# Kernel tuning notes

Measured on AMD Instinct MI355X. Metric: run time of the kernel, lower is better.

Reference implementation:

```python
import jax, jax.numpy as jnp
import numpy as np

N_NODES = 307
U = 100          # gru units / GAT out dim
D_IN = 3         # per-node input features
F_IN = U + D_IN  # 103, GATv2 input dim
NEG_SLOPE = 0.2


def setup_inputs() -> dict:
    key = jax.random.key(0)
    ks = jax.random.split(key, 12)
    B, E = 256, 4096
    inputs = jax.random.normal(ks[0], (B, N_NODES * D_IN), dtype=jnp.float32)
    state = jax.random.normal(ks[1], (B, N_NODES * U), dtype=jnp.float32)
    src = jax.random.randint(ks[2], (E,), 0, N_NODES, dtype=jnp.int32)
    dst = jax.random.randint(ks[3], (E,), 0, N_NODES, dtype=jnp.int32)
    def glorot(k, shape):
        lim = float(np.sqrt(6.0 / (shape[0] + shape[1])))
        return jax.random.uniform(k, shape, jnp.float32, -lim, lim)
    return {
        "inputs": inputs, "state": state, "src": src, "dst": dst,
        "Wl": glorot(ks[4], (F_IN, U)),        # GATv2 lin_l (source)
        "Wr": glorot(ks[5], (F_IN, U)),        # GATv2 lin_r (target)
        "att": jax.random.normal(ks[6], (U,), jnp.float32) * 0.1,
        "gat_bias": jnp.zeros((U,), jnp.float32),
        "bias_gc": jnp.zeros((U,), jnp.float32),   # self.bias_1 added in _gc3
        "W_gru1": glorot(ks[7], (F_IN, 2 * U)),    # GRULinear(100,200)
        "b_gru1": jnp.zeros((2 * U,), jnp.float32),
        "W_gru2": glorot(ks[8], (F_IN, U)),        # GRULinear(100,100)
        "b_gru2": jnp.zeros((U,), jnp.float32),
    }


def _gru_linear(inputs, hidden, W, b):
    # cat((inputs[B,N,3], hidden[B,N,U]), -1) @ W + b
    B = hidden.shape[0]
    x = jnp.concatenate([inputs.reshape(B, N_NODES, D_IN),
                         hidden.reshape(B, N_NODES, U)], axis=2)
    return jnp.einsum('bnf,fo->bno', x, W) + b


def _gatv2(x, src, dst, Wl, Wr, att, gat_bias):
    # x: (B, N, F_IN); PyG GATv2Conv with heads=1, add_self_loops=True
    loops = jnp.arange(N_NODES, dtype=src.dtype)
    s = jnp.concatenate([src, loops])
    d = jnp.concatenate([dst, loops])
    xl = jnp.einsum('bnf,fu->bnu', x, Wl)  # source transform
    xr = jnp.einsum('bnf,fu->bnu', x, Wr)  # target transform

    def per_sample(xl_b, xr_b):
        m = xl_b[s]                                        # (E', U)
        e = jax.nn.leaky_relu(m + xr_b[d], NEG_SLOPE) @ att  # (E',)
        emax = jax.ops.segment_max(e, d, num_segments=N_NODES)
        ex = jnp.exp(e - emax[d])
        denom = jax.ops.segment_sum(ex, d, num_segments=N_NODES)
        alpha = ex / denom[d]
        return jax.ops.segment_sum(alpha[:, None] * m, d, num_segments=N_NODES)

    out = jax.vmap(per_sample)(xl, xr)  # (B, N, U)
    return out + gat_bias


def reference(inputs, state, src, dst, Wl, Wr, att, gat_bias, bias_gc,
              W_gru1, b_gru1, W_gru2, b_gru2):
    B = state.shape[0]
    # _gc3: cat([state, inputs]) -> GATv2 per sample -> + bias_1
    x = jnp.concatenate([state.reshape(B, N_NODES, U),
                         inputs.reshape(B, N_NODES, D_IN)], axis=2)
    st = _gatv2(x, src, dst, Wl, Wr, att, gat_bias) + bias_gc
    st = st.reshape(B, N_NODES * U)
    # GRU gating
    value = jax.nn.sigmoid(_gru_linear(inputs, st, W_gru1, b_gru1))  # (B,N,2U)
    r, u = jnp.split(value, 2, axis=-1)
    r = r.reshape(B, N_NODES * U)
    u = u.reshape(B, N_NODES * U)
    c = jnp.tanh(_gru_linear(inputs, r * st, W_gru2, b_gru2)).reshape(B, N_NODES * U)
    return u * st + (1.0 - u) * c
```

## Files before the change

kernel.cpp:

```cpp
#include <hip/hip_runtime.h>
#include <math.h>

#define NN 307
#define UU 100
#define DD 3
#define UP 104
#define UNIT_W 14336
#define HCAP 2560
#define GT 1024
#define NGRP (GT / 16)
#define PACK_BLOCKS 280

typedef _Float16 f16;
typedef f16  f16x2 __attribute__((ext_vector_type(2)));
typedef f16  f16x4 __attribute__((ext_vector_type(4)));
typedef f16  f16x8 __attribute__((ext_vector_type(8)));
typedef float f32x4 __attribute__((ext_vector_type(4)));
typedef unsigned short u16;

__global__ __launch_bounds__(256)
void prep_k(const float* __restrict__ Wl, const float* __restrict__ Wr,
            const float* __restrict__ Wg1, const float* __restrict__ Wg2,
            f16* __restrict__ Wp,
            const int* __restrict__ dst, int E, int* offs)
{
    if (blockIdx.x < PACK_BLOCKS) {
        const int idx = blockIdx.x * 256 + threadIdx.x;
        const int u   = idx / UNIT_W;
        const int rem = idx - u * UNIT_W;
        const int e   = rem & 7;
        const int l   = (rem >> 3) & 63;
        const int sj  = rem >> 9;
        const int s   = sj / 7, j = sj - 7 * s;
        const int col = j * 16 + (l & 15);
        const int k   = (s * 4 + (l >> 4)) * 8 + e;
        float v = 0.f;
        if (col < UU && k < UU + DD) {
            if (u == 0)      v = Wl[k * UU + col];
            else if (u == 1) v = Wr[k * UU + col];
            else {
                const int kk = (k < UU) ? (k + DD) : (k - UU);
                if (u == 2)      v = Wg1[kk * (2 * UU) + col];
                else if (u == 3) v = Wg1[kk * (2 * UU) + UU + col];
                else             v = Wg2[kk * UU + col];
            }
        }
        Wp[idx] = (f16)v;
    } else {
        const int d = blockIdx.x - PACK_BLOCKS;
        if (threadIdx.x >= 64) return;
        const int lane = threadIdx.x;
        const int Etot = E + NN;
        int c = 0;
        for (int base = 0; base < Etot; base += 64) {
            const int e = base + lane;
            if (e < Etot) {
                const int de = (e < E) ? dst[e] : (e - E);
                c += (de == d) ? 1 : 0;
            }
        }
        #pragma unroll
        for (int m = 1; m < 64; m <<= 1) c += __shfl_xor(c, m, 64);
        if (lane == 0) {
            offs[d + 1] = c;
            if (d == 0) offs[0] = 0;
        }
    }
}

__global__ __launch_bounds__(512)
void csr_scan_k(int* offs)
{
    __shared__ int c[512];
    const int t = threadIdx.x;
    c[t] = (t < NN) ? offs[t + 1] : 0;
    __syncthreads();
    #pragma unroll
    for (int off = 1; off < 512; off <<= 1) {
        const int v = (t >= off) ? c[t - off] : 0;
        __syncthreads();
        c[t] += v;
        __syncthreads();
    }
    if (t < NN) offs[t + 1] = c[t];
    if (t == 0) offs[0] = 0;
}

__global__ __launch_bounds__(64)
void csr_fill_k(const int* __restrict__ src, const int* __restrict__ dst,
                int E, const int* __restrict__ offs,
                int* eidx, int* ddst)
{
    const int d = blockIdx.x;
    const int lane = threadIdx.x;
    const int Etot = E + NN;
    int w = offs[d];
    for (int base = 0; base < Etot; base += 64) {
        const int e = base + lane;
        bool match = false;
        int se = 0;
        if (e < Etot) {
            const int de = (e < E) ? dst[e] : (e - E);
            se           = (e < E) ? src[e] : (e - E);
            match = (de == d);
        }
        const unsigned long long mask = __ballot(match);
        if (match) {
            const int pos = w + __popcll(mask & ((1ULL << lane) - 1ULL));
            eidx[pos] = se;
            ddst[pos] = d;
        }
        w += __popcll(mask);
    }
}

__device__ __forceinline__ void mma_unit_nb(const f16x8 (&af)[4],
                                            const f16* __restrict__ Wu,
                                            int l, f32x4 (&acc)[7])
{
    #pragma unroll
    for (int s = 0; s < 4; ++s)
        #pragma unroll
        for (int j = 0; j < 7; ++j) {
            const f16x8 bv = *(const f16x8*)(Wu + (((s * 7 + j) * 64 + l) << 3));
            acc[j] = __builtin_amdgcn_mfma_f32_16x16x32_f16(af[s], bv, acc[j], 0, 0, 0);
        }
}

__device__ __forceinline__ void z7(f32x4 (&acc)[7])
{
    #pragma unroll
    for (int j = 0; j < 7; ++j) acc[j] = (f32x4)0.f;
}

__device__ __forceinline__ float fast_sigmoid(float x)
{
    return __fdividef(1.f, 1.f + __expf(-x));
}

__device__ __forceinline__ float fast_tanh(float x)
{
    return 1.f - __fdividef(2.f, __expf(2.f * x) + 1.f);
}

__global__ __launch_bounds__(256, 4)
void gemm_xlxr_k(const float* __restrict__ state, const float* __restrict__ inp,
                 const f16* __restrict__ Wp,
                 f16* __restrict__ xl, f16* __restrict__ xr, int M)
{
    const int tid = threadIdx.x;
    const int w = tid >> 6, l = tid & 63, lr = l & 15, lk = l >> 4;
    const int rb = blockIdx.x * 64 + w * 16;
    int crow = rb + lr; if (crow >= M) crow = M - 1;
    const float* bf = state + (size_t)crow * UU;

    f16x8 af[4];
    #pragma unroll
    for (int s = 0; s < 3; ++s) {
        const int kb = s * 4 + lk;
        const float4 x0 = *(const float4*)(bf + kb * 8);
        const float4 x1 = *(const float4*)(bf + kb * 8 + 4);
        f16x8 v;
        v[0]=(f16)x0.x; v[1]=(f16)x0.y; v[2]=(f16)x0.z; v[3]=(f16)x0.w;
        v[4]=(f16)x1.x; v[5]=(f16)x1.y; v[6]=(f16)x1.z; v[7]=(f16)x1.w;
        af[s] = v;
    }
    {
        f16x8 v = (f16x8)(f16)0.f;
        if (lk == 0) {
            const float4 x0 = *(const float4*)(bf + 96);
            v[0]=(f16)x0.x; v[1]=(f16)x0.y; v[2]=(f16)x0.z; v[3]=(f16)x0.w;
            v[4] = (f16)inp[(size_t)crow * DD + 0];
            v[5] = (f16)inp[(size_t)crow * DD + 1];
            v[6] = (f16)inp[(size_t)crow * DD + 2];
            v[7] = (f16)0.f;
        }
        af[3] = v;
    }

    #pragma unroll
    for (int u = 0; u < 2; ++u) {
        f32x4 acc[7];
        z7(acc);
        mma_unit_nb(af, Wp + (size_t)u * UNIT_W, l, acc);
        f16* dst = u ? xr : xl;
        #pragma unroll
        for (int j = 0; j < 7; ++j) {
            const int col = j * 16 + lr;
            if (col >= UU) continue;
            #pragma unroll
            for (int r = 0; r < 4; ++r) {
                const int row = rb + lk * 4 + r;
                if (row < M) dst[(size_t)row * UP + col] = (f16)acc[j][r];
            }
        }
    }
}

__global__ __launch_bounds__(GT, 8)
void gat2h_k(const f16* __restrict__ xl, const f16* __restrict__ xr,
             const int* __restrict__ offs, const int* __restrict__ eidx,
             const int* __restrict__ ddst,
             const float* __restrict__ att, const float* __restrict__ gb,
             const float* __restrict__ bgc,
             f16* __restrict__ stg)
{
    __shared__ f16   xl_s[NN * UP];
    __shared__ float sc_s[HCAP];
    __shared__ u16   ei_s[HCAP];
    __shared__ f16   att_s[UP];

    const int b   = blockIdx.x;
    const int h   = blockIdx.y;
    const int tid = threadIdx.x;
    const int d0 = h * 154;
    const int d1 = (h == 0) ? 154 : NN;
    const f16* xlb = xl + (size_t)b * NN * UP;
    const f16* xrb = xr + (size_t)b * NN * UP;
    f16* stb = stg + (size_t)b * NN * UP;

    if (tid < UP) att_s[tid] = (tid < UU) ? (f16)att[tid] : (f16)0.f;
    for (int c = tid; c < NN * UP / 8; c += GT)
        *(f16x8*)&xl_s[c * 8] = *(const f16x8*)&xlb[c * 8];

    int dlo = d0;
    while (dlo < d1) {
        int dhi = d1;
        const int base = offs[dlo];
        if (offs[d1] - base > HCAP) {
            int lo = dlo + 1, hi = d1;
            while (lo < hi) {
                const int mid = (lo + hi + 1) >> 1;
                if (offs[mid] - base <= HCAP) lo = mid; else hi = mid - 1;
            }
            dhi = lo;
        }
        const int e0 = base, e1 = offs[dhi];
        const int n  = e1 - e0;

        for (int q = tid; q < n; q += GT) ei_s[q] = (u16)eidx[e0 + q];
        __syncthreads();

        for (int i = tid; i < n; i += GT) {
            const int s = ei_s[i];
            const int d = ddst[e0 + i];
            const f16x8* a8 = (const f16x8*)&xl_s[s * UP];
            const f16x8* r8 = (const f16x8*)(xrb + (size_t)d * UP);
            float p0 = 0.f, p1 = 0.f;
            #pragma unroll 4
            for (int c = 0; c < 13; ++c) {
                const f16x8 x  = a8[c] + r8[c];
                const f16x8 xm = x * (f16)0.2f;
                const f16x8 y  = __builtin_elementwise_max(x, xm);
                const f16x2* y2  = (const f16x2*)&y;
                const f16x2* at2 = (const f16x2*)&att_s[c * 8];
#if __has_builtin(__builtin_amdgcn_fdot2)
                p0 = __builtin_amdgcn_fdot2(y2[0], at2[0], p0, false);
                p1 = __builtin_amdgcn_fdot2(y2[1], at2[1], p1, false);
                p0 = __builtin_amdgcn_fdot2(y2[2], at2[2], p0, false);
                p1 = __builtin_amdgcn_fdot2(y2[3], at2[3], p1, false);
#else
                #pragma unroll
                for (int q = 0; q < 4; ++q) {
                    p0 += (float)y2[q][0] * (float)at2[q][0];
                    p1 += (float)y2[q][1] * (float)at2[q][1];
                }
#endif
            }
            sc_s[i] = p0 + p1;
        }
        __syncthreads();

        {
            const int t = dlo + tid;
            if (t < dhi) {
                const int f0 = offs[t] - e0, f1 = offs[t + 1] - e0;
                float mx = -1e30f;
                for (int e = f0; e < f1; ++e) mx = fmaxf(mx, sc_s[e]);
                float dn = 0.f;
                for (int e = f0; e < f1; ++e) {
                    const float ex = __expf(sc_s[e] - mx);
                    sc_s[e] = ex;
                    dn += ex;
                }
                const float inv = 1.f / dn;
                for (int e = f0; e < f1; ++e) sc_s[e] *= inv;
            }
        }
        __syncthreads();

        {
            const int g   = tid >> 4;
            const int sub = tid & 15;
            const bool fa = (sub < 13);
            float bias_r[8];
            #pragma unroll
            for (int k = 0; k < 8; ++k) {
                const int f = sub * 8 + k;
                bias_r[k] = (fa && f < UU) ? (gb[f] + bgc[f]) : 0.f;
            }
            for (int d = dlo + g; d < dhi; d += NGRP) {
                const int f0 = offs[d] - e0, f1 = offs[d + 1] - e0;
                float acc[8] = {0.f, 0.f, 0.f, 0.f, 0.f, 0.f, 0.f, 0.f};
                for (int e = f0; e < f1; ++e) {
                    const float alpha = sc_s[e];
                    const int s = ei_s[e];
                    if (fa) {
                        const f16x8 m = *(const f16x8*)&xl_s[s * UP + sub * 8];
                        #pragma unroll
                        for (int k = 0; k < 8; ++k) acc[k] += alpha * (float)m[k];
                    }
                }
                if (fa) {
                    f16x8 o;
                    #pragma unroll
                    for (int k = 0; k < 8; ++k) o[k] = (f16)(acc[k] + bias_r[k]);
                    *(f16x8*)(stb + (size_t)d * UP + sub * 8) = o;
                }
            }
        }
        dlo = dhi;
        __syncthreads();
    }
}

__global__ __launch_bounds__(256, 6)
void gru3_k(const f16* __restrict__ st, const float* __restrict__ inp,
            const f16* __restrict__ Wp2 ,
            const float* __restrict__ bg1, const float* __restrict__ bg2,
            float* __restrict__ out, int M)
{
    __shared__ f16 st_s[64 * UP];
    __shared__ f16 rst_s[64 * UP];

    const int tid = threadIdx.x;
    const int w = tid >> 6, l = tid & 63, lr = l & 15, lk = l >> 4;
    const int rb = blockIdx.x * 64 + w * 16;
    const int lbase = w * 16;

    #pragma unroll
    for (int p = 0; p < 4; ++p) {
        const int idx = p * 64 + l;
        const int row = idx >> 4, ch = idx & 15;
        if (ch < 13) {
            int gr = rb + row; if (gr >= M) gr = M - 1;
            *(f16x8*)&st_s[(lbase + row) * UP + ch * 8] =
                *(const f16x8*)(st + (size_t)gr * UP + ch * 8);
        }
    }

    int crow = rb + lr; if (crow >= M) crow = M - 1;
    const f16* bh = &st_s[(lbase + lr) * UP];
    f16x8 af[4];
    #pragma unroll
    for (int s = 0; s < 3; ++s)
        af[s] = *(const f16x8*)(bh + (s * 4 + lk) * 8);
    {
        f16x8 v = (f16x8)(f16)0.f;
        if (lk == 0) {
            v = *(const f16x8*)(bh + 96);
            v[4] = (f16)inp[(size_t)crow * DD + 0];
            v[5] = (f16)inp[(size_t)crow * DD + 1];
            v[6] = (f16)inp[(size_t)crow * DD + 2];
            v[7] = (f16)0.f;
        }
        af[3] = v;
    }

    f32x4 acc[7];

    z7(acc);
    mma_unit_nb(af, Wp2, l, acc);
    #pragma unroll
    for (int j = 0; j < 7; ++j) {
        const int col = j * 16 + lr;
        if (col >= UU) continue;
        const float bR = bg1[col];
        #pragma unroll
        for (int r = 0; r < 4; ++r) {
            const int grow = rb + lk * 4 + r;
            const int lrow = lbase + lk * 4 + r;
            if (grow < M) {
                const float stv = (float)st_s[lrow * UP + col];
                const float sg = fast_sigmoid(acc[j][r] + bR);
                rst_s[lrow * UP + col] = (f16)(sg * stv);
            }
        }
    }
    if (l < 16) {
        const int grow2 = rb + l;
        const int lrow2 = lbase + l;
        if (grow2 < M) {
            rst_s[lrow2 * UP + 100] = (f16)inp[(size_t)grow2 * DD + 0];
            rst_s[lrow2 * UP + 101] = (f16)inp[(size_t)grow2 * DD + 1];
            rst_s[lrow2 * UP + 102] = (f16)inp[(size_t)grow2 * DD + 2];
            rst_s[lrow2 * UP + 103] = (f16)0.f;
        }
    }

    z7(acc);
    mma_unit_nb(af, Wp2 + UNIT_W, l, acc);
    f16x4 uh[7];
    #pragma unroll
    for (int j = 0; j < 7; ++j) {
        const int col = j * 16 + lr;
        const float bU = (col < UU) ? bg1[UU + col] : 0.f;
        #pragma unroll
        for (int r = 0; r < 4; ++r)
            uh[j][r] = (f16)fast_sigmoid(acc[j][r] + bU);
    }

    f16x8 af2[4];
    #pragma unroll
    for (int s = 0; s < 3; ++s)
        af2[s] = *(const f16x8*)&rst_s[(lbase + lr) * UP + (s * 4 + lk) * 8];
    af2[3] = (lk == 0) ? *(const f16x8*)&rst_s[(lbase + lr) * UP + 96]
                       : (f16x8)(f16)0.f;

    z7(acc);
    mma_unit_nb(af2, Wp2 + 2 * UNIT_W, l, acc);
    #pragma unroll
    for (int j = 0; j < 7; ++j) {
        const int col = j * 16 + lr;
        if (col >= UU) continue;
        const float bC = bg2[col];
        #pragma unroll
        for (int r = 0; r < 4; ++r) {
            const int grow = rb + lk * 4 + r;
            const int lrow = lbase + lk * 4 + r;
            if (grow < M) {
                const float c = fast_tanh(acc[j][r] + bC);
                const float u = (float)uh[j][r];
                const float stv = (float)st_s[lrow * UP + col];
                out[(size_t)grow * UU + col] = u * stv + (1.f - u) * c;
            }
        }
    }
}

extern "C" void kernel_launch(void* const* d_in, const int* in_sizes, int n_in,
                              void* d_out, int out_size, void* d_ws, size_t ws_size,
                              hipStream_t stream)
{
    const float* inputs   = (const float*)d_in[0];
    const float* state    = (const float*)d_in[1];
    const int*   src      = (const int*)  d_in[2];
    const int*   dst      = (const int*)  d_in[3];
    const float* Wl       = (const float*)d_in[4];
    const float* Wr       = (const float*)d_in[5];
    const float* att      = (const float*)d_in[6];
    const float* gat_bias = (const float*)d_in[7];
    const float* bias_gc  = (const float*)d_in[8];
    const float* Wg1      = (const float*)d_in[9];
    const float* bg1      = (const float*)d_in[10];
    const float* Wg2      = (const float*)d_in[11];
    const float* bg2      = (const float*)d_in[12];

    const int E = in_sizes[2];
    const int B = in_sizes[1] / (NN * UU);
    const int M = B * NN;
    const int Etot = E + NN;

    char* ws = (char*)d_ws;
    f16* Wp   = (f16*)ws;
    int* offs = (int*)(ws + 5 * UNIT_W * sizeof(f16));
    int* eidx = offs + (NN + 1);
    int* ddst = eidx + (Etot + 64);
    f16* xl_h = (f16*)(ws + (256 << 10));
    f16* xr_h = xl_h + (size_t)M * UP;
    f16* st_h = xr_h + (size_t)M * UP;
    float* out = (float*)d_out;

    prep_k<<<PACK_BLOCKS + NN, 256, 0, stream>>>(Wl, Wr, Wg1, Wg2, Wp,
                                                 dst, E, offs);
    csr_scan_k<<<1, 512, 0, stream>>>(offs);
    csr_fill_k<<<NN, 64, 0, stream>>>(src, dst, E, offs, eidx, ddst);

    gemm_xlxr_k<<<(M + 63) / 64, 256, 0, stream>>>(state, inputs, Wp,
                                                   xl_h, xr_h, M);

    gat2h_k<<<dim3(B, 2), GT, 0, stream>>>(xl_h, xr_h, offs, eidx, ddst,
                                           att, gat_bias, bias_gc, st_h);

    gru3_k<<<(M + 63) / 64, 256, 0, stream>>>(st_h, inputs,
        Wp + 2 * (size_t)UNIT_W, bg1, bg2, out, M);
}
```

Measured before the change: 148.6 us.

## Merge CSR scan, fill and xl/xr GEMM into a single heterogeneous kernel

Drops the separate single-block scan kernel. Each destination block now computes its own prefix offset by summing the per-destination counts in front of it. The CSR fill blocks and the xl/xr projection GEMM blocks are packed into one launch, so the graph build overlaps the GEMM and two kernel launches disappear. In exchange, every fill block does a redundant partial sum over up to 307 counts, and the CSR wave blocks share the launch with the 256-thread GEMM blocks, leaving 192 threads idle per CSR block.

```diff
diff --git a/kernel.cpp b/kernel.cpp
--- a/kernel.cpp
+++ b/kernel.cpp
@@ -22,7 +22,7 @@
 void prep_k(const float* __restrict__ Wl, const float* __restrict__ Wr,
             const float* __restrict__ Wg1, const float* __restrict__ Wg2,
             f16* __restrict__ Wp,
-            const int* __restrict__ dst, int E, int* offs)
+            const int* __restrict__ dst, int E, int* cnt)
 {
     if (blockIdx.x < PACK_BLOCKS) {
         const int idx = blockIdx.x * 256 + threadIdx.x;
@@ -61,56 +61,7 @@
         }
         #pragma unroll
         for (int m = 1; m < 64; m <<= 1) c += __shfl_xor(c, m, 64);
-        if (lane == 0) {
-            offs[d + 1] = c;
-            if (d == 0) offs[0] = 0;
-        }
-    }
-}
-
-__global__ __launch_bounds__(512)
-void csr_scan_k(int* offs)
-{
-    __shared__ int c[512];
-    const int t = threadIdx.x;
-    c[t] = (t < NN) ? offs[t + 1] : 0;
-    __syncthreads();
-    #pragma unroll
-    for (int off = 1; off < 512; off <<= 1) {
-        const int v = (t >= off) ? c[t - off] : 0;
-        __syncthreads();
-        c[t] += v;
-        __syncthreads();
-    }
-    if (t < NN) offs[t + 1] = c[t];
-    if (t == 0) offs[0] = 0;
-}
-
-__global__ __launch_bounds__(64)
-void csr_fill_k(const int* __restrict__ src, const int* __restrict__ dst,
-                int E, const int* __restrict__ offs,
-                int* eidx, int* ddst)
-{
-    const int d = blockIdx.x;
-    const int lane = threadIdx.x;
-    const int Etot = E + NN;
-    int w = offs[d];
-    for (int base = 0; base < Etot; base += 64) {
-        const int e = base + lane;
-        bool match = false;
-        int se = 0;
-        if (e < Etot) {
-            const int de = (e < E) ? dst[e] : (e - E);
-            se           = (e < E) ? src[e] : (e - E);
-            match = (de == d);
-        }
-        const unsigned long long mask = __ballot(match);
-        if (match) {
-            const int pos = w + __popcll(mask & ((1ULL << lane) - 1ULL));
-            eidx[pos] = se;
-            ddst[pos] = d;
-        }
-        w += __popcll(mask);
+        if (lane == 0) cnt[d] = c;
     }
 }
 
@@ -144,54 +95,90 @@
 }
 
 __global__ __launch_bounds__(256, 4)
-void gemm_xlxr_k(const float* __restrict__ state, const float* __restrict__ inp,
-                 const f16* __restrict__ Wp,
-                 f16* __restrict__ xl, f16* __restrict__ xr, int M)
-{
-    const int tid = threadIdx.x;
-    const int w = tid >> 6, l = tid & 63, lr = l & 15, lk = l >> 4;
-    const int rb = blockIdx.x * 64 + w * 16;
-    int crow = rb + lr; if (crow >= M) crow = M - 1;
-    const float* bf = state + (size_t)crow * UU;
-
-    f16x8 af[4];
-    #pragma unroll
-    for (int s = 0; s < 3; ++s) {
-        const int kb = s * 4 + lk;
-        const float4 x0 = *(const float4*)(bf + kb * 8);
-        const float4 x1 = *(const float4*)(bf + kb * 8 + 4);
-        f16x8 v;
-        v[0]=(f16)x0.x; v[1]=(f16)x0.y; v[2]=(f16)x0.z; v[3]=(f16)x0.w;
-        v[4]=(f16)x1.x; v[5]=(f16)x1.y; v[6]=(f16)x1.z; v[7]=(f16)x1.w;
-        af[s] = v;
-    }
-    {
-        f16x8 v = (f16x8)(f16)0.f;
-        if (lk == 0) {
-            const float4 x0 = *(const float4*)(bf + 96);
+void mid_k(const int* __restrict__ src, const int* __restrict__ dst, int E,
+           const int* __restrict__ cnt, int* __restrict__ offs,
+           int* __restrict__ eidx, int* __restrict__ ddst,
+           const float* __restrict__ state, const float* __restrict__ inp,
+           const f16* __restrict__ Wp,
+           f16* __restrict__ xl, f16* __restrict__ xr, int M)
+{
+    if (blockIdx.x < NN) {
+        const int d = blockIdx.x;
+        if (threadIdx.x >= 64) return;
+        const int lane = threadIdx.x;
+        int base = 0;
+        for (int i = lane; i < d; i += 64) base += cnt[i];
+        #pragma unroll
+        for (int m = 1; m < 64; m <<= 1) base += __shfl_xor(base, m, 64);
+        if (lane == 0) {
+            offs[d + 1] = base + cnt[d];
+            if (d == 0) offs[0] = 0;
+        }
+        const int Etot = E + NN;
+        int w = base;
+        for (int eb = 0; eb < Etot; eb += 64) {
+            const int e = eb + lane;
+            bool match = false;
+            int se = 0;
+            if (e < Etot) {
+                const int de = (e < E) ? dst[e] : (e - E);
+                se           = (e < E) ? src[e] : (e - E);
+                match = (de == d);
+            }
+            const unsigned long long mask = __ballot(match);
+            if (match) {
+                const int pos = w + __popcll(mask & ((1ULL << lane) - 1ULL));
+                eidx[pos] = se;
+                ddst[pos] = d;
+            }
+            w += __popcll(mask);
+        }
+    } else {
+        const int tid = threadIdx.x;
+        const int w = tid >> 6, l = tid & 63, lr = l & 15, lk = l >> 4;
+        const int rb = (blockIdx.x - NN) * 64 + w * 16;
+        int crow = rb + lr; if (crow >= M) crow = M - 1;
+        const float* bf = state + (size_t)crow * UU;
+
+        f16x8 af[4];
+        #pragma unroll
+        for (int s = 0; s < 3; ++s) {
+            const int kb = s * 4 + lk;
+            const float4 x0 = *(const float4*)(bf + kb * 8);
+            const float4 x1 = *(const float4*)(bf + kb * 8 + 4);
+            f16x8 v;
             v[0]=(f16)x0.x; v[1]=(f16)x0.y; v[2]=(f16)x0.z; v[3]=(f16)x0.w;
-            v[4] = (f16)inp[(size_t)crow * DD + 0];
-            v[5] = (f16)inp[(size_t)crow * DD + 1];
-            v[6] = (f16)inp[(size_t)crow * DD + 2];
-            v[7] = (f16)0.f;
-        }
-        af[3] = v;
-    }
-
-    #pragma unroll
-    for (int u = 0; u < 2; ++u) {
-        f32x4 acc[7];
-        z7(acc);
-        mma_unit_nb(af, Wp + (size_t)u * UNIT_W, l, acc);
-        f16* dst = u ? xr : xl;
-        #pragma unroll
-        for (int j = 0; j < 7; ++j) {
-            const int col = j * 16 + lr;
-            if (col >= UU) continue;
+            v[4]=(f16)x1.x; v[5]=(f16)x1.y; v[6]=(f16)x1.z; v[7]=(f16)x1.w;
+            af[s] = v;
+        }
+        {
+            f16x8 v = (f16x8)(f16)0.f;
+            if (lk == 0) {
+                const float4 x0 = *(const float4*)(bf + 96);
+                v[0]=(f16)x0.x; v[1]=(f16)x0.y; v[2]=(f16)x0.z; v[3]=(f16)x0.w;
+                v[4] = (f16)inp[(size_t)crow * DD + 0];
+                v[5] = (f16)inp[(size_t)crow * DD + 1];
+                v[6] = (f16)inp[(size_t)crow * DD + 2];
+                v[7] = (f16)0.f;
+            }
+            af[3] = v;
+        }
+
+        #pragma unroll
+        for (int u = 0; u < 2; ++u) {
+            f32x4 acc[7];
+            z7(acc);
+            mma_unit_nb(af, Wp + (size_t)u * UNIT_W, l, acc);
+            f16* dstp = u ? xr : xl;
             #pragma unroll
-            for (int r = 0; r < 4; ++r) {
-                const int row = rb + lk * 4 + r;
-                if (row < M) dst[(size_t)row * UP + col] = (f16)acc[j][r];
+            for (int j = 0; j < 7; ++j) {
+                const int col = j * 16 + lr;
+                if (col >= UU) continue;
+                #pragma unroll
+                for (int r = 0; r < 4; ++r) {
+                    const int row = rb + lk * 4 + r;
+                    if (row < M) dstp[(size_t)row * UP + col] = (f16)acc[j][r];
+                }
             }
         }
     }
@@ -460,11 +447,13 @@
     const int B = in_sizes[1] / (NN * UU);
     const int M = B * NN;
     const int Etot = E + NN;
+    const int mb = (M + 63) / 64;
 
     char* ws = (char*)d_ws;
     f16* Wp   = (f16*)ws;
     int* offs = (int*)(ws + 5 * UNIT_W * sizeof(f16));
-    int* eidx = offs + (NN + 1);
+    int* cnt  = offs + (NN + 1);
+    int* eidx = cnt + NN;
     int* ddst = eidx + (Etot + 64);
     f16* xl_h = (f16*)(ws + (256 << 10));
     f16* xr_h = xl_h + (size_t)M * UP;
@@ -472,16 +461,11 @@
     float* out = (float*)d_out;
 
     prep_k<<<PACK_BLOCKS + NN, 256, 0, stream>>>(Wl, Wr, Wg1, Wg2, Wp,
-                                                 dst, E, offs);
-    csr_scan_k<<<1, 512, 0, stream>>>(offs);
-    csr_fill_k<<<NN, 64, 0, stream>>>(src, dst, E, offs, eidx, ddst);
-
-    gemm_xlxr_k<<<(M + 63) / 64, 256, 0, stream>>>(state, inputs, Wp,
-                                                   xl_h, xr_h, M);
-
+                                                 dst, E, cnt);
+    mid_k<<<NN + mb, 256, 0, stream>>>(src, dst, E, cnt, offs, eidx, ddst,
+                                       state, inputs, Wp, xl_h, xr_h, M);
     gat2h_k<<<dim3(B, 2), GT, 0, stream>>>(xl_h, xr_h, offs, eidx, ddst,
                                            att, gat_bias, bias_gc, st_h);
-
-    gru3_k<<<(M + 63) / 64, 256, 0, stream>>>(st_h, inputs,
+    gru3_k<<<mb, 256, 0, stream>>>(st_h, inputs,
         Wp + 2 * (size_t)UNIT_W, bg1, bg2, out, M);
 }
```

Result: faster. 134.0 us (-9.9%).
